# Optimization experiments

Hardware: AMD Instinct MI355X
Metric: run time of the kernel (lower is better)

The kernel has to match this reference:

```python
import jax, jax.numpy as jnp
import numpy as np

N_NODES = 150000
N_EDGES = 2400000


def setup_inputs() -> dict:
    key = jax.random.key(0)
    ks = jax.random.split(key, 7)
    x = jax.random.normal(ks[0], (N_NODES, 9), dtype=jnp.float32)
    edge_index = jax.random.randint(ks[1], (2, N_EDGES), 0, N_NODES, dtype=jnp.int32)
    edge_weight = jax.random.uniform(ks[2], (N_EDGES,), dtype=jnp.float32, minval=0.1, maxval=1.0)
    W1 = jax.random.normal(ks[3], (9, 32), dtype=jnp.float32) * (1.0 / np.sqrt(9))
    b1 = jnp.zeros((32,), dtype=jnp.float32)
    W2 = jax.random.normal(ks[4], (32, 7), dtype=jnp.float32) * (1.0 / np.sqrt(32))
    b2 = jnp.zeros((7,), dtype=jnp.float32)
    return {"x": x, "edge_index": edge_index, "edge_weight": edge_weight,
            "W1": W1, "b1": b1, "W2": W2, "b2": b2}


def gcn_norm(edge_index, edge_weight, num_nodes):
    # PyG gcn_norm: add self-loops (weight 1), symmetric D^-1/2 A D^-1/2
    row, col = edge_index[0], edge_index[1]
    loop = jnp.arange(num_nodes, dtype=edge_index.dtype)
    row = jnp.concatenate([row, loop])
    col = jnp.concatenate([col, loop])
    w = jnp.concatenate([edge_weight, jnp.ones((num_nodes,), edge_weight.dtype)])
    deg = jax.ops.segment_sum(w, col, num_segments=num_nodes)  # [N]
    dinv = jnp.where(deg > 0, jax.lax.rsqrt(deg), 0.0)
    norm = dinv[row] * w * dinv[col]  # [E+N]
    return row, col, norm


def gcn_conv(x, W, b, row, col, norm, num_nodes):
    h = x @ W                                   # [N, out]
    msg = norm[:, None] * h[row]                # [E+N, out] gather + scale
    out = jax.ops.segment_sum(msg, col, num_segments=num_nodes)  # scatter-add
    return out + b


def reference(x, edge_index, edge_weight, W1, b1, W2, b2):
    n = x.shape[0]
    row, col, norm = gcn_norm(edge_index, edge_weight, n)
    h = jax.nn.relu(gcn_conv(x, W1, b1, row, col, norm, n))
    # dropout is identity in eval mode
    h = gcn_conv(h, W2, b2, row, col, norm, n)
    return jax.nn.log_softmax(h, axis=1)
```

## Files before the change

### kernel.cpp

```cpp
#include <hip/hip_runtime.h>

constexpr int F_IN  = 9;
constexpr int F_HID = 32;
constexpr int F_OUT = 7;

constexpr int SB_SHIFT = 13;
constexpr int SB_NODES = 1 << SB_SHIFT;
constexpr int NSB      = 19;
constexpr int SB_CAP   = 135424;
constexpr int A_EDGES  = 2048;
constexpr int FB_PER_SB= SB_NODES / 256;
constexpr int NBKT     = 586;
constexpr int NBKT_PAD = NSB * FB_PER_SB;
constexpr int BCAP     = 4864;
constexpr int B_EDGES  = 4096;
constexpr int B_CHUNKS = (SB_CAP + B_EDGES - 1) / B_EDGES;
constexpr int ROW_MASK = (1 << 18) - 1;

__device__ __forceinline__ int2 nt_load_int2(const int2* p) {
    long long v = __builtin_nontemporal_load(reinterpret_cast<const long long*>(p));
    return make_int2((int)(v & 0xffffffffLL), (int)((unsigned long long)v >> 32));
}

__global__ void k_zcur(int* __restrict__ bcur) {
    int i = blockIdx.x * 256 + threadIdx.x;
    if (i < NBKT_PAD) bcur[i * 16] = i * BCAP;
}

__global__ __launch_bounds__(256) void k_histA(
    const int* __restrict__ col, int* __restrict__ ghist, int nblkA, int E)
{
    __shared__ int h[NSB];
    const int tid = threadIdx.x;
    if (tid < NSB) h[tid] = 0;
    __syncthreads();
    const int t0 = blockIdx.x * A_EDGES;
    const int kend = min(A_EDGES, E - t0);
    for (int k = tid; k < kend; k += 256)
        atomicAdd(&h[col[t0 + k] >> SB_SHIFT], 1);
    __syncthreads();
    if (tid < NSB) ghist[(size_t)tid * nblkA + blockIdx.x] = h[tid];
}

__global__ __launch_bounds__(256) void k_scanA(
    int* __restrict__ ghist, int* __restrict__ sbcnt, int nblkA)
{
    __shared__ int sc[256];
    const int s = blockIdx.x, tid = threadIdx.x;
    int* r = ghist + (size_t)s * nblkA;
    const int per = (nblkA + 255) / 256;
    const int i0 = tid * per, i1 = min(i0 + per, nblkA);

    int sum = 0;
    for (int i = i0; i < i1; ++i) sum += r[i];
    sc[tid] = sum; __syncthreads();
    for (int d = 1; d < 256; d <<= 1) {
        int u = (tid >= d) ? sc[tid - d] : 0;
        __syncthreads();
        sc[tid] += u; __syncthreads();
    }
    int run = sc[tid] - sum;
    for (int i = i0; i < i1; ++i) { int v = r[i]; r[i] = run; run += v; }
    if (tid == 255) sbcnt[s] = run;
}

__global__ __launch_bounds__(256) void k_scatA(
    const int* __restrict__ row, const int* __restrict__ col,
    const float* __restrict__ w, const int* __restrict__ ghist,
    int2* __restrict__ sbrec, int nblkA, int E)
{
    __shared__ int rb[NSB];
    __shared__ int cur[NSB];
    const int b = blockIdx.x, tid = threadIdx.x;
    if (tid < NSB) {
        rb[tid] = tid * SB_CAP + ghist[(size_t)tid * nblkA + b];
        cur[tid] = 0;
    }
    __syncthreads();
    const int t0 = b * A_EDGES;
    const int kend = min(A_EDGES, E - t0);
    for (int k = tid; k < kend; k += 256) {
        int e = t0 + k;
        int c = col[e];
        int s = c >> SB_SHIFT;
        int2 rec = make_int2(row[e] | ((c & (SB_NODES - 1)) << 18),
                             __float_as_int(w[e]));
        int rk = atomicAdd(&cur[s], 1);
        int pos = rb[s] + rk;
        if (pos < (s + 1) * SB_CAP)
            sbrec[pos] = rec;
    }
}

__global__ __launch_bounds__(256) void k_fbkt(
    const int2* __restrict__ sbrec, const int* __restrict__ sbcnt,
    int* __restrict__ bcur, int2* __restrict__ irec)
{
    __shared__ int2 s_rec[B_EDGES];
    __shared__ int hist[FB_PER_SB * 4];
    __shared__ int rbase[FB_PER_SB * 4];

    const int sb    = blockIdx.x / B_CHUNKS;
    const int chunk = blockIdx.x % B_CHUNKS;
    const int cnt   = min(sbcnt[sb], SB_CAP);
    const int k0    = chunk * B_EDGES;
    const int kend  = min(B_EDGES, cnt - k0);
    if (kend <= 0) return;

    const int tid = threadIdx.x, wv = tid >> 6;
    for (int i = tid; i < FB_PER_SB * 4; i += 256) hist[i] = 0;
    __syncthreads();

    const int base = sb * SB_CAP + k0;
    for (int k = tid; k < kend; k += 256) {
        int2 rc = sbrec[base + k];
        s_rec[k] = rc;
        int fb = ((unsigned)rc.x >> 18) >> 8;
        atomicAdd(&hist[fb * 4 + wv], 1);
    }
    __syncthreads();
    for (int i = tid; i < FB_PER_SB * 4; i += 256) {
        int c = hist[i];
        int gb = sb * FB_PER_SB + (i >> 2);
        rbase[i] = c ? atomicAdd(&bcur[gb * 16], c) : 0;
        hist[i] = 0;
    }
    __syncthreads();
    for (int k = tid; k < kend; k += 256) {
        int2 rc = s_rec[k];
        int fb = ((unsigned)rc.x >> 18) >> 8;
        int idx = fb * 4 + wv;
        int rk = atomicAdd(&hist[idx], 1);
        int pos = rbase[idx] + rk;
        int gb = sb * FB_PER_SB + fb;
        if (pos < (gb + 1) * BCAP)
            irec[pos] = rc;
    }
}

__global__ __launch_bounds__(256) void k_sortbucket(
    int2* __restrict__ irec, const int* __restrict__ bcur,
    const float* __restrict__ x, int4* __restrict__ meta,
    float* __restrict__ xd, int N)
{
    __shared__ int2  s_rec[BCAP];
    __shared__ int   hist[256];
    __shared__ float wsum[256];
    __shared__ int   nbase[256];
    __shared__ int   scur[256];
    __shared__ float sdinv[256];

    const int b    = blockIdx.x;
    const int tid  = threadIdx.x;
    const int base = b * BCAP;
    const int cnt  = min(bcur[b * 16] - base, BCAP);

    hist[tid] = 0; wsum[tid] = 0.0f; scur[tid] = 0;
    __syncthreads();

    for (int k = tid; k < cnt; k += 256) {
        int2 rc = irec[base + k];
        s_rec[k] = rc;
        int c = ((unsigned)rc.x >> 18) & 255;
        atomicAdd(&hist[c], 1);
        atomicAdd(&wsum[c], __int_as_float(rc.y));
    }
    __syncthreads();

    int v = hist[tid];
    nbase[tid] = v;
    __syncthreads();
    for (int d = 1; d < 256; d <<= 1) {
        int u = (tid >= d) ? nbase[tid - d] : 0;
        __syncthreads();
        nbase[tid] += u;
        __syncthreads();
    }
    int excl = nbase[tid] - v;
    __syncthreads();
    nbase[tid] = excl;

    int node = b * 256 + tid;
    float dv = rsqrtf(1.0f + wsum[tid]);
    sdinv[tid] = dv;
    if (node < N)
        meta[node] = make_int4(base + excl, v, __float_as_int(dv), 0);
    __syncthreads();

    int nnode = min(256, N - b * 256);
    if (nnode > 0) {
        int tot = nnode * F_IN;
        size_t gbase = (size_t)(b * 256) * F_IN;
        for (int i = tid; i < tot; i += 256)
            xd[gbase + i] = sdinv[i / F_IN] * x[gbase + i];
    }

    for (int k = tid; k < cnt; k += 256) {
        int2 rc = s_rec[k];
        int c = ((unsigned)rc.x >> 18) & 255;
        int r = atomicAdd(&scur[c], 1);
        irec[base + nbase[c] + r] = make_int2(rc.x & ROW_MASK, rc.y);
    }
}

__global__ __launch_bounds__(256) void k_g1mlp(
    const int2* __restrict__ csr, const int4* __restrict__ meta,
    const float* __restrict__ xd,
    const float* __restrict__ W1, const float* __restrict__ b1,
    const float* __restrict__ W2, float* __restrict__ h2d, int N)
{
    __shared__ float sW1[F_IN * F_HID];
    __shared__ float sb1[F_HID];
    __shared__ float sW2[F_HID * F_OUT];
    for (int t = threadIdx.x; t < F_IN * F_HID; t += 256) sW1[t] = W1[t];
    for (int t = threadIdx.x; t < F_HID;        t += 256) sb1[t] = b1[t];
    for (int t = threadIdx.x; t < F_HID * F_OUT; t += 256) sW2[t] = W2[t];
    __syncthreads();

    int t   = blockIdx.x * 256 + threadIdx.x;
    int i   = t >> 2;
    int sub = t & 3;
    if (i >= N) return;
    int4 m = meta[i];
    float dv = __int_as_float(m.z);

    float acc[F_IN];
    if (sub == 0) {
        #pragma unroll
        for (int j = 0; j < F_IN; ++j) acc[j] = xd[(size_t)i * F_IN + j];
    } else {
        #pragma unroll
        for (int j = 0; j < F_IN; ++j) acc[j] = 0.0f;
    }
    int s = m.x, tend = m.x + m.y;
    for (int e = s + sub; e < tend; e += 4) {
        int2 pr = nt_load_int2(&csr[e]);
        const float* xr = xd + (size_t)pr.x * F_IN;
        float wv = __int_as_float(pr.y);
        #pragma unroll
        for (int j = 0; j < F_IN; ++j) acc[j] = fmaf(wv, xr[j], acc[j]);
    }
    #pragma unroll
    for (int d = 1; d < 4; d <<= 1) {
        #pragma unroll
        for (int j = 0; j < F_IN; ++j)
            acc[j] += __shfl_xor(acc[j], d, 4);
    }
    #pragma unroll
    for (int j = 0; j < F_IN; ++j) acc[j] *= dv;

    float o[F_OUT];
    #pragma unroll
    for (int c = 0; c < F_OUT; ++c) o[c] = 0.0f;
    int ks = sub * 8;
    #pragma unroll
    for (int k = 0; k < 8; ++k) {
        float hk = sb1[ks + k];
        #pragma unroll
        for (int j = 0; j < F_IN; ++j) hk = fmaf(acc[j], sW1[j * F_HID + ks + k], hk);
        hk = fmaxf(hk, 0.0f);
        #pragma unroll
        for (int c = 0; c < F_OUT; ++c) o[c] = fmaf(hk, sW2[(ks + k) * F_OUT + c], o[c]);
    }
    #pragma unroll
    for (int d = 1; d < 4; d <<= 1) {
        #pragma unroll
        for (int c = 0; c < F_OUT; ++c)
            o[c] += __shfl_xor(o[c], d, 4);
    }
    for (int c = sub; c < F_OUT; c += 4)
        h2d[(size_t)i * F_OUT + c] = dv * o[c];
}

__global__ __launch_bounds__(256) void k_g2ls(
    const int2* __restrict__ csr, const int4* __restrict__ meta,
    const float* __restrict__ h2d, const float* __restrict__ b2,
    float* __restrict__ out, int N)
{
    int t   = blockIdx.x * 256 + threadIdx.x;
    int i   = t >> 2;
    int sub = t & 3;
    if (i >= N) return;
    int4 m = meta[i];
    float dv = __int_as_float(m.z);

    float acc[F_OUT];
    if (sub == 0) {
        #pragma unroll
        for (int c = 0; c < F_OUT; ++c) acc[c] = h2d[(size_t)i * F_OUT + c];
    } else {
        #pragma unroll
        for (int c = 0; c < F_OUT; ++c) acc[c] = 0.0f;
    }
    int s = m.x, tend = m.x + m.y;
    for (int e = s + sub; e < tend; e += 4) {
        int2 pr = nt_load_int2(&csr[e]);
        const float* hr = h2d + (size_t)pr.x * F_OUT;
        float wv = __int_as_float(pr.y);
        #pragma unroll
        for (int c = 0; c < F_OUT; ++c) acc[c] = fmaf(wv, hr[c], acc[c]);
    }
    #pragma unroll
    for (int d = 1; d < 4; d <<= 1) {
        #pragma unroll
        for (int c = 0; c < F_OUT; ++c)
            acc[c] += __shfl_xor(acc[c], d, 4);
    }

    float vv[F_OUT];
    float mx = -1e30f;
    #pragma unroll
    for (int c = 0; c < F_OUT; ++c) {
        vv[c] = dv * acc[c] + b2[c];
        mx = fmaxf(mx, vv[c]);
    }
    float ss = 0.0f;
    #pragma unroll
    for (int c = 0; c < F_OUT; ++c) ss += __expf(vv[c] - mx);
    float ls = __logf(ss);
    for (int c = sub; c < F_OUT; c += 4)
        out[(size_t)i * F_OUT + c] = vv[c] - mx - ls;
}

extern "C" void kernel_launch(void* const* d_in, const int* in_sizes, int n_in,
                              void* d_out, int out_size, void* d_ws, size_t ws_size,
                              hipStream_t stream) {
    const float* x  = (const float*)d_in[0];
    const int*   ei = (const int*)  d_in[1];
    const float* ew = (const float*)d_in[2];
    const float* W1 = (const float*)d_in[3];
    const float* b1 = (const float*)d_in[4];
    const float* W2 = (const float*)d_in[5];
    const float* b2 = (const float*)d_in[6];
    float* out = (float*)d_out;

    const int N = in_sizes[0] / F_IN;
    const int E = in_sizes[2];
    const int* row = ei;
    const int* col = ei + E;
    const int nblkA = (E + A_EDGES - 1) / A_EDGES;

    int2* sbrec = (int2*)d_ws;
    int2* irec  = sbrec + (size_t)NSB * SB_CAP;
    int*  bcur  = (int*)(irec + (size_t)NBKT * BCAP);
    int*  ghist = bcur + (size_t)NBKT_PAD * 16;
    int*  sbcnt = ghist + (size_t)NSB * nblkA;
    int4*  meta = (int4*)d_ws;
    float* xd   = (float*)(meta + N);
    float* h2d  = xd + (size_t)N * F_IN;

    const int gB = NSB * B_CHUNKS;
    const int gN4 = (4 * N + 255) / 256;

    k_zcur      <<<(NBKT_PAD + 255) / 256, 256, 0, stream>>>(bcur);
    k_histA     <<<nblkA, 256, 0, stream>>>(col, ghist, nblkA, E);
    k_scanA     <<<NSB, 256, 0, stream>>>(ghist, sbcnt, nblkA);
    k_scatA     <<<nblkA, 256, 0, stream>>>(row, col, ew, ghist, sbrec, nblkA, E);
    k_fbkt      <<<gB, 256, 0, stream>>>(sbrec, sbcnt, bcur, irec);
    k_sortbucket<<<NBKT, 256, 0, stream>>>(irec, bcur, x, meta, xd, N);
    k_g1mlp     <<<gN4, 256, 0, stream>>>(irec, meta, xd, W1, b1, W2, h2d, N);
    k_g2ls      <<<gN4, 256, 0, stream>>>(irec, meta, h2d, b2, out, N);
}
```

Measured before the change: 160.3 us.

## Pack CSR edges into 32-bit row+weight and store node features as fp16

The sorted CSR record shrinks from an int2 (row, float weight) to one 32-bit word: an 18-bit row index plus a 14-bit fixed-point weight. The scaled input features and the layer-2 intermediate are stored as packed fp16 pairs, padded to 5 and 4 words per node. Both aggregation kernels unpack these values and accumulate in fp32. The goal is to cut the memory traffic of the random gathers and CSR streaming, at the cost of extra rounding error that could exceed tolerance. The packed CSR is also written in place over the int2 buffer that other buckets may still be reading, which is a possible race.

```diff
diff --git a/kernel.cpp b/kernel.cpp
--- a/kernel.cpp
+++ b/kernel.cpp
@@ -1,4 +1,5 @@
 #include <hip/hip_runtime.h>
+#include <hip/hip_fp16.h>
 
 constexpr int F_IN  = 9;
 constexpr int F_HID = 32;
@@ -17,9 +18,17 @@
 constexpr int B_CHUNKS = (SB_CAP + B_EDGES - 1) / B_EDGES;
 constexpr int ROW_MASK = (1 << 18) - 1;
 
-__device__ __forceinline__ int2 nt_load_int2(const int2* p) {
-    long long v = __builtin_nontemporal_load(reinterpret_cast<const long long*>(p));
-    return make_int2((int)(v & 0xffffffffLL), (int)((unsigned long long)v >> 32));
+__device__ __forceinline__ int nt_load_int(const int* p) {
+    return __builtin_nontemporal_load(p);
+}
+
+__device__ __forceinline__ unsigned pack_h2(float a, float b) {
+    return (unsigned)__half_as_ushort(__float2half(a)) |
+           ((unsigned)__half_as_ushort(__float2half(b)) << 16);
+}
+__device__ __forceinline__ float2 unpack_h2(unsigned u) {
+    return make_float2(__half2float(__ushort_as_half((unsigned short)(u & 0xffffu))),
+                       __half2float(__ushort_as_half((unsigned short)(u >> 16))));
 }
 
 __global__ void k_zcur(int* __restrict__ bcur) {
@@ -139,9 +148,9 @@
 }
 
 __global__ __launch_bounds__(256) void k_sortbucket(
-    int2* __restrict__ irec, const int* __restrict__ bcur,
-    const float* __restrict__ x, int4* __restrict__ meta,
-    float* __restrict__ xd, int N)
+    int2* __restrict__ irec, int* __restrict__ csr4,
+    const int* __restrict__ bcur, const float* __restrict__ x,
+    int4* __restrict__ meta, unsigned* __restrict__ xdh, int N)
 {
     __shared__ int2  s_rec[BCAP];
     __shared__ int   hist[256];
@@ -187,27 +196,33 @@
         meta[node] = make_int4(base + excl, v, __float_as_int(dv), 0);
     __syncthreads();
 
-    int nnode = min(256, N - b * 256);
-    if (nnode > 0) {
-        int tot = nnode * F_IN;
-        size_t gbase = (size_t)(b * 256) * F_IN;
-        for (int i = tid; i < tot; i += 256)
-            xd[gbase + i] = sdinv[i / F_IN] * x[gbase + i];
+    if (node < N) {
+        float xv[F_IN];
+        #pragma unroll
+        for (int j = 0; j < F_IN; ++j) xv[j] = dv * x[(size_t)node * F_IN + j];
+        size_t o = (size_t)node * 5;
+        xdh[o + 0] = pack_h2(xv[0], xv[1]);
+        xdh[o + 1] = pack_h2(xv[2], xv[3]);
+        xdh[o + 2] = pack_h2(xv[4], xv[5]);
+        xdh[o + 3] = pack_h2(xv[6], xv[7]);
+        xdh[o + 4] = pack_h2(xv[8], 0.0f);
     }
 
     for (int k = tid; k < cnt; k += 256) {
         int2 rc = s_rec[k];
         int c = ((unsigned)rc.x >> 18) & 255;
         int r = atomicAdd(&scur[c], 1);
-        irec[base + nbase[c] + r] = make_int2(rc.x & ROW_MASK, rc.y);
+        float wf = __int_as_float(rc.y);
+        int wq = min((int)(wf * 16384.0f + 0.5f), 16383);
+        csr4[base + nbase[c] + r] = ((rc.x & ROW_MASK) << 14) | wq;
     }
 }
 
 __global__ __launch_bounds__(256) void k_g1mlp(
-    const int2* __restrict__ csr, const int4* __restrict__ meta,
-    const float* __restrict__ xd,
+    const int* __restrict__ csr4, const int4* __restrict__ meta,
+    const unsigned* __restrict__ xdh,
     const float* __restrict__ W1, const float* __restrict__ b1,
-    const float* __restrict__ W2, float* __restrict__ h2d, int N)
+    const float* __restrict__ W2, unsigned* __restrict__ h2dh, int N)
 {
     __shared__ float sW1[F_IN * F_HID];
     __shared__ float sb1[F_HID];
@@ -225,20 +240,31 @@
     float dv = __int_as_float(m.z);
 
     float acc[F_IN];
+    #pragma unroll
+    for (int j = 0; j < F_IN; ++j) acc[j] = 0.0f;
     if (sub == 0) {
-        #pragma unroll
-        for (int j = 0; j < F_IN; ++j) acc[j] = xd[(size_t)i * F_IN + j];
-    } else {
-        #pragma unroll
-        for (int j = 0; j < F_IN; ++j) acc[j] = 0.0f;
+        size_t o = (size_t)i * 5;
+        #pragma unroll
+        for (int p = 0; p < 5; ++p) {
+            float2 f = unpack_h2(xdh[o + p]);
+            acc[2 * p] = f.x;
+            if (2 * p + 1 < F_IN) acc[2 * p + 1] = f.y;
+        }
     }
     int s = m.x, tend = m.x + m.y;
     for (int e = s + sub; e < tend; e += 4) {
-        int2 pr = nt_load_int2(&csr[e]);
-        const float* xr = xd + (size_t)pr.x * F_IN;
-        float wv = __int_as_float(pr.y);
-        #pragma unroll
-        for (int j = 0; j < F_IN; ++j) acc[j] = fmaf(wv, xr[j], acc[j]);
+        int v = nt_load_int(&csr4[e]);
+        int r = (int)((unsigned)v >> 14);
+        float wv = (float)(v & 16383) * (1.0f / 16384.0f);
+        size_t o = (size_t)r * 5;
+        unsigned u0 = xdh[o], u1 = xdh[o+1], u2 = xdh[o+2], u3 = xdh[o+3], u4 = xdh[o+4];
+        float2 f0 = unpack_h2(u0), f1 = unpack_h2(u1), f2 = unpack_h2(u2),
+               f3 = unpack_h2(u3), f4 = unpack_h2(u4);
+        acc[0] = fmaf(wv, f0.x, acc[0]); acc[1] = fmaf(wv, f0.y, acc[1]);
+        acc[2] = fmaf(wv, f1.x, acc[2]); acc[3] = fmaf(wv, f1.y, acc[3]);
+        acc[4] = fmaf(wv, f2.x, acc[4]); acc[5] = fmaf(wv, f2.y, acc[5]);
+        acc[6] = fmaf(wv, f3.x, acc[6]); acc[7] = fmaf(wv, f3.y, acc[7]);
+        acc[8] = fmaf(wv, f4.x, acc[8]);
     }
     #pragma unroll
     for (int d = 1; d < 4; d <<= 1) {
@@ -268,13 +294,14 @@
         for (int c = 0; c < F_OUT; ++c)
             o[c] += __shfl_xor(o[c], d, 4);
     }
-    for (int c = sub; c < F_OUT; c += 4)
-        h2d[(size_t)i * F_OUT + c] = dv * o[c];
+    float pa = dv * o[2 * sub];
+    float pb = (2 * sub + 1 < F_OUT) ? dv * o[2 * sub + 1] : 0.0f;
+    h2dh[(size_t)i * 4 + sub] = pack_h2(pa, pb);
 }
 
 __global__ __launch_bounds__(256) void k_g2ls(
-    const int2* __restrict__ csr, const int4* __restrict__ meta,
-    const float* __restrict__ h2d, const float* __restrict__ b2,
+    const int* __restrict__ csr4, const int4* __restrict__ meta,
+    const unsigned* __restrict__ h2dh, const float* __restrict__ b2,
     float* __restrict__ out, int N)
 {
     int t   = blockIdx.x * 256 + threadIdx.x;
@@ -285,20 +312,27 @@
     float dv = __int_as_float(m.z);
 
     float acc[F_OUT];
+    #pragma unroll
+    for (int c = 0; c < F_OUT; ++c) acc[c] = 0.0f;
     if (sub == 0) {
-        #pragma unroll
-        for (int c = 0; c < F_OUT; ++c) acc[c] = h2d[(size_t)i * F_OUT + c];
-    } else {
-        #pragma unroll
-        for (int c = 0; c < F_OUT; ++c) acc[c] = 0.0f;
+        uint4 h4 = *reinterpret_cast<const uint4*>(h2dh + (size_t)i * 4);
+        float2 f0 = unpack_h2(h4.x), f1 = unpack_h2(h4.y),
+               f2 = unpack_h2(h4.z), f3 = unpack_h2(h4.w);
+        acc[0] = f0.x; acc[1] = f0.y; acc[2] = f1.x; acc[3] = f1.y;
+        acc[4] = f2.x; acc[5] = f2.y; acc[6] = f3.x;
     }
     int s = m.x, tend = m.x + m.y;
     for (int e = s + sub; e < tend; e += 4) {
-        int2 pr = nt_load_int2(&csr[e]);
-        const float* hr = h2d + (size_t)pr.x * F_OUT;
-        float wv = __int_as_float(pr.y);
-        #pragma unroll
-        for (int c = 0; c < F_OUT; ++c) acc[c] = fmaf(wv, hr[c], acc[c]);
+        int v = nt_load_int(&csr4[e]);
+        int r = (int)((unsigned)v >> 14);
+        float wv = (float)(v & 16383) * (1.0f / 16384.0f);
+        uint4 h4 = *reinterpret_cast<const uint4*>(h2dh + (size_t)r * 4);
+        float2 f0 = unpack_h2(h4.x), f1 = unpack_h2(h4.y),
+               f2 = unpack_h2(h4.z), f3 = unpack_h2(h4.w);
+        acc[0] = fmaf(wv, f0.x, acc[0]); acc[1] = fmaf(wv, f0.y, acc[1]);
+        acc[2] = fmaf(wv, f1.x, acc[2]); acc[3] = fmaf(wv, f1.y, acc[3]);
+        acc[4] = fmaf(wv, f2.x, acc[4]); acc[5] = fmaf(wv, f2.y, acc[5]);
+        acc[6] = fmaf(wv, f3.x, acc[6]);
     }
     #pragma unroll
     for (int d = 1; d < 4; d <<= 1) {
@@ -342,12 +376,13 @@
 
     int2* sbrec = (int2*)d_ws;
     int2* irec  = sbrec + (size_t)NSB * SB_CAP;
+    int*  csr4  = (int*)irec;
     int*  bcur  = (int*)(irec + (size_t)NBKT * BCAP);
     int*  ghist = bcur + (size_t)NBKT_PAD * 16;
     int*  sbcnt = ghist + (size_t)NSB * nblkA;
-    int4*  meta = (int4*)d_ws;
-    float* xd   = (float*)(meta + N);
-    float* h2d  = xd + (size_t)N * F_IN;
+    int4*     meta = (int4*)d_ws;
+    unsigned* xdh  = (unsigned*)(meta + N);
+    unsigned* h2dh = xdh + (size_t)N * 5;
 
     const int gB = NSB * B_CHUNKS;
     const int gN4 = (4 * N + 255) / 256;
@@ -357,7 +392,7 @@
     k_scanA     <<<NSB, 256, 0, stream>>>(ghist, sbcnt, nblkA);
     k_scatA     <<<nblkA, 256, 0, stream>>>(row, col, ew, ghist, sbrec, nblkA, E);
     k_fbkt      <<<gB, 256, 0, stream>>>(sbrec, sbcnt, bcur, irec);
-    k_sortbucket<<<NBKT, 256, 0, stream>>>(irec, bcur, x, meta, xd, N);
-    k_g1mlp     <<<gN4, 256, 0, stream>>>(irec, meta, xd, W1, b1, W2, h2d, N);
-    k_g2ls      <<<gN4, 256, 0, stream>>>(irec, meta, h2d, b2, out, N);
-}
+    k_sortbucket<<<NBKT, 256, 0, stream>>>(irec, csr4, bcur, x, meta, xdh, N);
+    k_g1mlp     <<<gN4, 256, 0, stream>>>(csr4, meta, xdh, W1, b1, W2, h2dh, N);
+    k_g2ls      <<<gN4, 256, 0, stream>>>(csr4, meta, h2dh, b2, out, N);
+}
```

New measurement: 133.8 us. 16.6% less time.
